# Kernel optimization log

Measured on AMD Instinct MI355X. Metric: run time of the kernel, lower is better.

Reference implementation:

```python
import jax, jax.numpy as jnp
import numpy as np


def setup_inputs() -> dict:
    key = jax.random.key(0)
    kq, kk, kw, kv = jax.random.split(key, 4)
    B, T, Dq, Dk, A = 32, 4096, 512, 512, 512
    q = jax.random.normal(kq, (B, Dq), dtype=jnp.float32)
    k = jax.random.normal(kk, (B, T, Dk), dtype=jnp.float32)
    # Dense kernel over concat([q, k]) last dim -> attention_size (TruncatedNormal 0.02)
    W = jax.random.truncated_normal(kw, -2.0, 2.0, (Dq + Dk, A), dtype=jnp.float32) * 0.02
    b = jnp.zeros((A,), dtype=jnp.float32)
    # VarianceScaling(scale=2.0, 'normal') over fan_in=A
    v = jax.random.normal(kv, (A,), dtype=jnp.float32) * jnp.sqrt(2.0 / A)
    return {"q": q, "k": k, "W": W, "b": b, "v": v}


def reference(q, k, W, b, v):
    # Original: tile q over T, concat with k, Dense(tanh), dot with v.
    # Equivalent (same math) without materializing the [B,T,Dq+Dk] concat:
    # split W into Wq (rows for q part) and Wk (rows for k part).
    Dq = q.shape[-1]
    Wq, Wk = W[:Dq], W[Dq:]
    qp = q @ Wq                                  # [B, A]
    kp = jnp.einsum('btd,da->bta', k, Wk)        # [B, T, A]
    out = jnp.tanh(qp[:, None, :] + kp + b)      # [B, T, A]
    score = jnp.einsum('bta,a->bt', out, v)      # [B, T]
    return score
```

## Files before the change

kernel.cpp:

```cpp
#include <hip/hip_runtime.h>
#include <hip/hip_bf16.h>
#include <stdint.h>

#define DQ 512
#define DK 512
#define NA 512
#define TT 4096
#define NBATCH 32
#define M_TOTAL (NBATCH * TT)

#define BM 128
#define BN 128
#define BK 32

typedef __attribute__((ext_vector_type(8))) short bf16x8;
typedef __attribute__((ext_vector_type(4))) float f32x4;

__device__ __forceinline__ void gll16(const void* g, void* l) {
  __builtin_amdgcn_global_load_lds(
      (const __attribute__((address_space(1))) uint32_t*)g,
      (__attribute__((address_space(3))) uint32_t*)l, 16, 0, 0);
}

__device__ __forceinline__ float fast_tanh(float x) {
  float e = __expf(2.0f * x);
  return 1.0f - 2.0f * __builtin_amdgcn_rcpf(e + 1.0f);
}

__global__ void prep_kernel(const float* __restrict__ W,
                            __hip_bfloat16* __restrict__ WkT,
                            float* __restrict__ out) {
  int i = blockIdx.x * 256 + threadIdx.x;
  int d = i & (DK - 1);
  int a = i >> 9;
  WkT[i] = __float2bfloat16(W[(size_t)(DQ + d) * NA + a]);
  if (i < M_TOTAL) out[i] = 0.0f;
}

__global__ void qpb_kernel(const float* __restrict__ q,
                           const float* __restrict__ W,
                           const float* __restrict__ bias,
                           float* __restrict__ qpb) {
  int b = blockIdx.x;
  int a = threadIdx.x;
  const float* qr = q + b * DQ;
  float acc = bias[a];
#pragma unroll 16
  for (int d = 0; d < DQ; ++d)
    acc = fmaf(qr[d], W[(size_t)d * NA + a], acc);
  qpb[b * NA + a] = acc;
}

__global__ __launch_bounds__(256)
void score_kernel(const float* __restrict__ Kmat,
                  const __hip_bfloat16* __restrict__ WkT,
                  const float* __restrict__ qpb,
                  const float* __restrict__ v,
                  float* __restrict__ out) {
  __shared__ __align__(16) __hip_bfloat16 As[BM * BK];
  __shared__ __align__(16) __hip_bfloat16 Bs[BN * BK];

  const int tid  = threadIdx.x;
  const int lane = tid & 63;
  const int w    = tid >> 6;
  const int wm   = w >> 1;
  const int wn   = w & 1;
  const int r16  = lane & 15;
  const int quad = lane >> 4;

  const int n_tile = blockIdx.x & 3;
  const int m_tile = blockIdx.x >> 2;

  const float* Ag = Kmat + (size_t)m_tile * BM * DK;
  const __hip_bfloat16* Bg = WkT + (size_t)n_tile * BN * DK;

  f32x4 acc[4][4];
#pragma unroll
  for (int i = 0; i < 4; ++i)
#pragma unroll
    for (int j = 0; j < 4; ++j) {
      f32x4 z = {0.0f, 0.0f, 0.0f, 0.0f};
      acc[i][j] = z;
    }

  for (int kk = 0; kk < DK; kk += BK) {
    __syncthreads();

#pragma unroll
    for (int j = 0; j < 2; ++j) {
      const int s  = j * 256 + tid;
      const int s0 = j * 256 + w * 64;
      const __hip_bfloat16* src = Bg + (size_t)(s >> 2) * DK + kk + (s & 3) * 8;
      gll16((const void*)src, (void*)((char*)Bs + (size_t)s0 * 16));
    }

#pragma unroll
    for (int j = 0; j < 2; ++j) {
      const int c   = j * 256 + tid;
      const int row = c >> 2;
      const int kp  = (c & 3) * 8;
      const float* src = Ag + (size_t)row * DK + kk + kp;
      float4 f0 = *(const float4*)(src);
      float4 f1 = *(const float4*)(src + 4);
      union { bf16x8 v8; __hip_bfloat16 h[8]; } u;
      u.h[0] = __float2bfloat16(f0.x);
      u.h[1] = __float2bfloat16(f0.y);
      u.h[2] = __float2bfloat16(f0.z);
      u.h[3] = __float2bfloat16(f0.w);
      u.h[4] = __float2bfloat16(f1.x);
      u.h[5] = __float2bfloat16(f1.y);
      u.h[6] = __float2bfloat16(f1.z);
      u.h[7] = __float2bfloat16(f1.w);
      *(bf16x8*)(As + row * BK + kp) = u.v8;
    }

    __syncthreads();

    const bf16x8* Av = (const bf16x8*)As;
    const bf16x8* Bv = (const bf16x8*)Bs;
    bf16x8 af[4], bfr[4];
#pragma unroll
    for (int ms = 0; ms < 4; ++ms)
      af[ms] = Av[(wm * 64 + ms * 16 + r16) * 4 + quad];
#pragma unroll
    for (int ns = 0; ns < 4; ++ns)
      bfr[ns] = Bv[(wn * 64 + ns * 16 + r16) * 4 + quad];
#pragma unroll
    for (int ms = 0; ms < 4; ++ms)
#pragma unroll
      for (int ns = 0; ns < 4; ++ns)
        acc[ms][ns] = __builtin_amdgcn_mfma_f32_16x16x32_bf16(
            af[ms], bfr[ns], acc[ms][ns], 0, 0, 0);
  }

  const size_t row0 = (size_t)m_tile * BM + wm * 64;
  const int b_idx = (int)(row0 >> 12);
  const int a0 = n_tile * BN + wn * 64;

  float vv[4], qv[4];
#pragma unroll
  for (int ns = 0; ns < 4; ++ns) {
    int a = a0 + ns * 16 + r16;
    vv[ns] = v[a];
    qv[ns] = qpb[b_idx * NA + a];
  }

#pragma unroll
  for (int ms = 0; ms < 4; ++ms) {
#pragma unroll
    for (int reg = 0; reg < 4; ++reg) {
      float sum = 0.0f;
#pragma unroll
      for (int ns = 0; ns < 4; ++ns) {
        float x = acc[ms][ns][reg] + qv[ns];
        sum = fmaf(fast_tanh(x), vv[ns], sum);
      }
      sum += __shfl_xor(sum, 1);
      sum += __shfl_xor(sum, 2);
      sum += __shfl_xor(sum, 4);
      sum += __shfl_xor(sum, 8);
      if (r16 == 0)
        atomicAdd(&out[row0 + ms * 16 + quad * 4 + reg], sum);
    }
  }
}

extern "C" void kernel_launch(void* const* d_in, const int* in_sizes, int n_in,
                              void* d_out, int out_size, void* d_ws, size_t ws_size,
                              hipStream_t stream) {
  const float* q  = (const float*)d_in[0];
  const float* k  = (const float*)d_in[1];
  const float* W  = (const float*)d_in[2];
  const float* b  = (const float*)d_in[3];
  const float* v  = (const float*)d_in[4];
  float* out = (float*)d_out;

  float* qpb = (float*)d_ws;
  __hip_bfloat16* WkT = (__hip_bfloat16*)((char*)d_ws + 65536);

  prep_kernel<<<(NA * DK) / 256, 256, 0, stream>>>(W, WkT, out);
  qpb_kernel<<<NBATCH, NA, 0, stream>>>(q, W, b, qpb);
  score_kernel<<<(M_TOTAL / BM) * (NA / BN), 256, 0, stream>>>(k, WkT, qpb, v, out);
}
```

Before: 479.5 us.

## Cover full attention dim per block, drop atomics, tile-transpose Wk in prep

The score kernel now gives each block a 64-row tile that spans all 512 attention columns. Each K row is therefore read and converted from fp32 once instead of four times, and the atomicAdd reduction into out is replaced by an LDS partial-sum reduction followed by a single plain store, so out no longer needs zeroing. The A-tile global load is issued before the first barrier to overlap with the B loads, and a cheaper bit-trick fp32-to-bf16 pack is used (round-half-up rather than round-to-nearest-even). The prep transpose now goes through an LDS tile for coalesced access, and qpb is launched with more, smaller blocks. In exchange the accumulator doubles to 128 floats per thread, the B tile grows fourfold per iteration, and occupancy may drop.

```diff
diff --git a/kernel.cpp b/kernel.cpp
--- a/kernel.cpp
+++ b/kernel.cpp
@@ -9,9 +9,10 @@
 #define NBATCH 32
 #define M_TOTAL (NBATCH * TT)
 
-#define BM 128
-#define BN 128
+#define BM 64
+#define BN 512
 #define BK 32
+#define KITERS (DK / BK)
 
 typedef __attribute__((ext_vector_type(8))) short bf16x8;
 typedef __attribute__((ext_vector_type(4))) float f32x4;
@@ -22,125 +23,135 @@
       (__attribute__((address_space(3))) uint32_t*)l, 16, 0, 0);
 }
 
+__device__ __forceinline__ uint32_t pack2bf16(float a, float b) {
+  uint32_t ua = __float_as_uint(a) + 0x8000u;
+  uint32_t ub = __float_as_uint(b) + 0x8000u;
+  return __builtin_amdgcn_perm(ub, ua, 0x07060302);
+}
+
 __device__ __forceinline__ float fast_tanh(float x) {
   float e = __expf(2.0f * x);
   return 1.0f - 2.0f * __builtin_amdgcn_rcpf(e + 1.0f);
 }
 
 __global__ void prep_kernel(const float* __restrict__ W,
-                            __hip_bfloat16* __restrict__ WkT,
-                            float* __restrict__ out) {
-  int i = blockIdx.x * 256 + threadIdx.x;
-  int d = i & (DK - 1);
-  int a = i >> 9;
-  WkT[i] = __float2bfloat16(W[(size_t)(DQ + d) * NA + a]);
-  if (i < M_TOTAL) out[i] = 0.0f;
+                            uint16_t* __restrict__ WkT) {
+  __shared__ uint16_t T[64][65];
+  const int tid = threadIdx.x;
+  const int d0 = (blockIdx.x & 7) * 64;
+  const int a0 = (blockIdx.x >> 3) * 64;
+#pragma unroll
+  for (int j = 0; j < 16; ++j) {
+    int dd = j * 4 + (tid >> 6);
+    int aa = tid & 63;
+    uint32_t u = __float_as_uint(W[(size_t)(DQ + d0 + dd) * NA + a0 + aa]) + 0x8000u;
+    T[dd][aa] = (uint16_t)(u >> 16);
+  }
+  __syncthreads();
+#pragma unroll
+  for (int j = 0; j < 8; ++j) {
+    int aa = j * 8 + (tid >> 5);
+    int dp = (tid & 31) * 2;
+    uint32_t val = (uint32_t)T[dp][aa] | ((uint32_t)T[dp + 1][aa] << 16);
+    *(uint32_t*)(WkT + (size_t)(a0 + aa) * DK + d0 + dp) = val;
+  }
 }
 
 __global__ void qpb_kernel(const float* __restrict__ q,
                            const float* __restrict__ W,
                            const float* __restrict__ bias,
                            float* __restrict__ qpb) {
-  int b = blockIdx.x;
-  int a = threadIdx.x;
+  int b = blockIdx.x >> 3;
+  int a = (blockIdx.x & 7) * 64 + threadIdx.x;
   const float* qr = q + b * DQ;
   float acc = bias[a];
-#pragma unroll 16
+#pragma unroll 8
   for (int d = 0; d < DQ; ++d)
     acc = fmaf(qr[d], W[(size_t)d * NA + a], acc);
   qpb[b * NA + a] = acc;
 }
 
-__global__ __launch_bounds__(256)
+__global__ __launch_bounds__(256, 2)
 void score_kernel(const float* __restrict__ Kmat,
-                  const __hip_bfloat16* __restrict__ WkT,
+                  const uint16_t* __restrict__ WkT,
                   const float* __restrict__ qpb,
                   const float* __restrict__ v,
                   float* __restrict__ out) {
-  __shared__ __align__(16) __hip_bfloat16 As[BM * BK];
-  __shared__ __align__(16) __hip_bfloat16 Bs[BN * BK];
+  __shared__ __align__(16) uint16_t As[BM * BK];
+  __shared__ __align__(16) uint16_t Bs[BN * BK];
+  __shared__ float part[4][BM];
 
   const int tid  = threadIdx.x;
   const int lane = tid & 63;
   const int w    = tid >> 6;
-  const int wm   = w >> 1;
-  const int wn   = w & 1;
   const int r16  = lane & 15;
   const int quad = lane >> 4;
-
-  const int n_tile = blockIdx.x & 3;
-  const int m_tile = blockIdx.x >> 2;
+  const int m_tile = blockIdx.x;
 
   const float* Ag = Kmat + (size_t)m_tile * BM * DK;
-  const __hip_bfloat16* Bg = WkT + (size_t)n_tile * BN * DK;
 
-  f32x4 acc[4][4];
+  f32x4 acc[4][8];
 #pragma unroll
   for (int i = 0; i < 4; ++i)
 #pragma unroll
-    for (int j = 0; j < 4; ++j) {
-      f32x4 z = {0.0f, 0.0f, 0.0f, 0.0f};
+    for (int j = 0; j < 8; ++j) {
+      f32x4 z = {0.f, 0.f, 0.f, 0.f};
       acc[i][j] = z;
     }
 
-  for (int kk = 0; kk < DK; kk += BK) {
+  const int arow = tid >> 2;
+  const int akp  = (tid & 3) * 8;
+  const float* Asrc = Ag + (size_t)arow * DK + akp;
+  uint16_t* Adst = As + arow * BK + akp;
+
+  for (int it = 0; it < KITERS; ++it) {
+    const int kk = it * BK;
+    float4 f0 = *(const float4*)(Asrc + kk);
+    float4 f1 = *(const float4*)(Asrc + kk + 4);
+
     __syncthreads();
 
 #pragma unroll
-    for (int j = 0; j < 2; ++j) {
-      const int s  = j * 256 + tid;
-      const int s0 = j * 256 + w * 64;
-      const __hip_bfloat16* src = Bg + (size_t)(s >> 2) * DK + kk + (s & 3) * 8;
-      gll16((const void*)src, (void*)((char*)Bs + (size_t)s0 * 16));
+    for (int j = 0; j < 8; ++j) {
+      const int g0 = j * 256 + w * 64;
+      const int g  = g0 + lane;
+      const uint16_t* src = WkT + (size_t)(g >> 2) * DK + kk + (g & 3) * 8;
+      gll16((const void*)src, (void*)((char*)Bs + (size_t)g0 * 16));
     }
 
-#pragma unroll
-    for (int j = 0; j < 2; ++j) {
-      const int c   = j * 256 + tid;
-      const int row = c >> 2;
-      const int kp  = (c & 3) * 8;
-      const float* src = Ag + (size_t)row * DK + kk + kp;
-      float4 f0 = *(const float4*)(src);
-      float4 f1 = *(const float4*)(src + 4);
-      union { bf16x8 v8; __hip_bfloat16 h[8]; } u;
-      u.h[0] = __float2bfloat16(f0.x);
-      u.h[1] = __float2bfloat16(f0.y);
-      u.h[2] = __float2bfloat16(f0.z);
-      u.h[3] = __float2bfloat16(f0.w);
-      u.h[4] = __float2bfloat16(f1.x);
-      u.h[5] = __float2bfloat16(f1.y);
-      u.h[6] = __float2bfloat16(f1.z);
-      u.h[7] = __float2bfloat16(f1.w);
-      *(bf16x8*)(As + row * BK + kp) = u.v8;
-    }
+    uint4 p;
+    p.x = pack2bf16(f0.x, f0.y);
+    p.y = pack2bf16(f0.z, f0.w);
+    p.z = pack2bf16(f1.x, f1.y);
+    p.w = pack2bf16(f1.z, f1.w);
+    *(uint4*)Adst = p;
 
     __syncthreads();
 
     const bf16x8* Av = (const bf16x8*)As;
     const bf16x8* Bv = (const bf16x8*)Bs;
-    bf16x8 af[4], bfr[4];
+    bf16x8 af[4], bfr[8];
 #pragma unroll
     for (int ms = 0; ms < 4; ++ms)
-      af[ms] = Av[(wm * 64 + ms * 16 + r16) * 4 + quad];
+      af[ms] = Av[(ms * 16 + r16) * 4 + quad];
 #pragma unroll
-    for (int ns = 0; ns < 4; ++ns)
-      bfr[ns] = Bv[(wn * 64 + ns * 16 + r16) * 4 + quad];
+    for (int ns = 0; ns < 8; ++ns)
+      bfr[ns] = Bv[(w * 128 + ns * 16 + r16) * 4 + quad];
 #pragma unroll
     for (int ms = 0; ms < 4; ++ms)
 #pragma unroll
-      for (int ns = 0; ns < 4; ++ns)
+      for (int ns = 0; ns < 8; ++ns)
         acc[ms][ns] = __builtin_amdgcn_mfma_f32_16x16x32_bf16(
             af[ms], bfr[ns], acc[ms][ns], 0, 0, 0);
   }
 
-  const size_t row0 = (size_t)m_tile * BM + wm * 64;
-  const int b_idx = (int)(row0 >> 12);
-  const int a0 = n_tile * BN + wn * 64;
+  const size_t row0 = (size_t)m_tile * BM;
+  const int b_idx = m_tile >> 6;
 
-  float vv[4], qv[4];
+  float vv[8], qv[8];
 #pragma unroll
-  for (int ns = 0; ns < 4; ++ns) {
-    int a = a0 + ns * 16 + r16;
+  for (int ns = 0; ns < 8; ++ns) {
+    int a = w * 128 + ns * 16 + r16;
     vv[ns] = v[a];
     qv[ns] = qpb[b_idx * NA + a];
   }
@@ -149,36 +160,38 @@
   for (int ms = 0; ms < 4; ++ms) {
 #pragma unroll
     for (int reg = 0; reg < 4; ++reg) {
-      float sum = 0.0f;
+      float s = 0.f;
 #pragma unroll
-      for (int ns = 0; ns < 4; ++ns) {
+      for (int ns = 0; ns < 8; ++ns) {
         float x = acc[ms][ns][reg] + qv[ns];
-        sum = fmaf(fast_tanh(x), vv[ns], sum);
+        s = fmaf(fast_tanh(x), vv[ns], s);
       }
-      sum += __shfl_xor(sum, 1);
-      sum += __shfl_xor(sum, 2);
-      sum += __shfl_xor(sum, 4);
-      sum += __shfl_xor(sum, 8);
-      if (r16 == 0)
-        atomicAdd(&out[row0 + ms * 16 + quad * 4 + reg], sum);
+      s += __shfl_xor(s, 1);
+      s += __shfl_xor(s, 2);
+      s += __shfl_xor(s, 4);
+      s += __shfl_xor(s, 8);
+      if (r16 == 0) part[w][ms * 16 + quad * 4 + reg] = s;
     }
   }
+  __syncthreads();
+  if (tid < BM)
+    out[row0 + tid] = part[0][tid] + part[1][tid] + part[2][tid] + part[3][tid];
 }
 
 extern "C" void kernel_launch(void* const* d_in, const int* in_sizes, int n_in,
                               void* d_out, int out_size, void* d_ws, size_t ws_size,
                               hipStream_t stream) {
-  const float* q  = (const float*)d_in[0];
-  const float* k  = (const float*)d_in[1];
-  const float* W  = (const float*)d_in[2];
-  const float* b  = (const float*)d_in[3];
-  const float* v  = (const float*)d_in[4];
+  const float* q = (const float*)d_in[0];
+  const float* k = (const float*)d_in[1];
+  const float* W = (const float*)d_in[2];
+  const float* b = (const float*)d_in[3];
+  const float* v = (const float*)d_in[4];
   float* out = (float*)d_out;
 
   float* qpb = (float*)d_ws;
-  __hip_bfloat16* WkT = (__hip_bfloat16*)((char*)d_ws + 65536);
+  uint16_t* WkT = (uint16_t*)((char*)d_ws + 65536);
 
-  prep_kernel<<<(NA * DK) / 256, 256, 0, stream>>>(W, WkT, out);
-  qpb_kernel<<<NBATCH, NA, 0, stream>>>(q, W, b, qpb);
-  score_kernel<<<(M_TOTAL / BM) * (NA / BN), 256, 0, stream>>>(k, WkT, qpb, v, out);
+  prep_kernel<<<64, 256, 0, stream>>>(W, WkT);
+  qpb_kernel<<<256, 64, 0, stream>>>(q, W, b, qpb);
+  score_kernel<<<M_TOTAL / BM, 256, 0, stream>>>(k, WkT, qpb, v, out);
 }
```

Result: no change. 476.4 us (-0.6%).
